# Kernel tuning notes

Hardware: AMD Instinct MI355X
Metric: run time of the kernel (lower is better)

## Reference

```python
import math
import jax, jax.numpy as jnp
import numpy as np

H = 8  # num_heads

def _layernorm(x, scale, bias, eps=1e-5):
    m = x.mean(-1, keepdims=True)
    v = x.var(-1, keepdims=True)
    return (x - m) / jnp.sqrt(v + eps) * scale + bias

def setup_inputs() -> dict:
    key = jax.random.key(0)
    ks = jax.random.split(key, 12)
    B, C, P, D, G = 8, 32, 256, 256, 512
    n = jax.random.normal
    return {
        "qz": n(ks[0], (B, C, P, D), dtype=jnp.float32),
        "unary": n(ks[1], (B, C, P, D), dtype=jnp.float32),
        # per-sample condition-instantiated factors; scaled ~1/sqrt(D) so attn logits are sane
        "time_u": n(ks[2], (B, D, D), dtype=jnp.float32) * 0.06,
        "time_v": n(ks[3], (B, D, D), dtype=jnp.float32) * 0.06,
        "channel_u": n(ks[4], (B, D, D), dtype=jnp.float32) * 0.06,
        "channel_v": n(ks[5], (B, D, D), dtype=jnp.float32) * 0.06,
        "topic_binary": n(ks[6], (B, G, D), dtype=jnp.float32) * 0.02,
        "norm_scale": jnp.ones((D,), jnp.float32),
        "norm_bias": jnp.zeros((D,), jnp.float32),
        "gate_w": n(ks[7], (D, D), dtype=jnp.float32) * 0.02,
        "gate_b": jnp.zeros((D,), jnp.float32),
        "out_w1": n(ks[8], (D, D), dtype=jnp.float32) * 0.02,
        "out_b1": jnp.zeros((D,), jnp.float32),
        "out_w2": n(ks[9], (D, D), dtype=jnp.float32) * 0.02,
        "out_b2": jnp.zeros((D,), jnp.float32),
    }

def reference(qz, unary, time_u, time_v, channel_u, channel_v, topic_binary,
              norm_scale, norm_bias, gate_w, gate_b, out_w1, out_b1, out_w2, out_b2):
    B, C, P, D = qz.shape
    R = D // H
    inv_sqrt_r = 1.0 / math.sqrt(R)

    qz_n = _layernorm(qz, norm_scale, norm_bias)

    def heads(x, w):  # [B,C,P,D] x [B,D,D] -> [B,C,P,H,R]
        return jnp.einsum('bcpd,bod->bcpo', x, w).reshape(B, C, P, H, R)

    # --- time-factor message: attention over P within each (b, c, h) ---
    qu = heads(qz_n, time_u).transpose(0, 1, 3, 2, 4)   # [B,C,H,P,R]
    qv = heads(qz_n, time_v).transpose(0, 1, 3, 2, 4)
    attn_t = jax.nn.softmax(jnp.einsum('bchpr,bchqr->bchpq', qu, qv) * inv_sqrt_r, axis=-1)
    m_t = jnp.einsum('bchpq,bcqd->bchpd', attn_t, qz_n).mean(axis=2)  # [B,C,P,D]

    # --- channel-factor message: attention over C within each (b, p, h) ---
    qu = heads(qz_n, channel_u).transpose(0, 2, 3, 1, 4)  # [B,P,H,C,R]
    qv = heads(qz_n, channel_v).transpose(0, 2, 3, 1, 4)
    attn_c = jax.nn.softmax(jnp.einsum('bphcr,bphfr->bphcf', qu, qv) * inv_sqrt_r, axis=-1)
    qzp = qz_n.transpose(0, 2, 1, 3)                      # [B,P,C,D]
    m_c = jnp.einsum('bphcf,bpfd->bphcd', attn_c, qzp).mean(axis=2).transpose(0, 2, 1, 3)

    # --- topic-modeling binary factor with AbsNormalize (relu + L1-normalize) ---
    qg = jax.nn.relu(jnp.einsum('bcpd,bgd->bcpg', qz_n, topic_binary))
    qg = qg / jnp.maximum(qg.sum(axis=-1, keepdims=True), 1e-6)
    m_g = jnp.einsum('bcpg,bgd->bcpd', qg, topic_binary)

    # --- gated residual update ---
    gate = jax.nn.sigmoid(qz @ gate_w.T + gate_b)
    qz2 = gate * qz + (1.0 - gate) * (unary + m_t + m_c + m_g)

    # --- output MLP with shared LayerNorm ---
    h = _layernorm(qz2, norm_scale, norm_bias)
    h = jax.nn.gelu(h @ out_w1.T + out_b1, approximate=False) @ out_w2.T + out_b2
    return qz2 + h
```

## Files before the change

### kernel.cpp

```cpp
#include <hip/hip_runtime.h>
#include <math.h>

namespace {

constexpr float INV_SQRT_R = 0.17677669529663689f;

typedef __attribute__((ext_vector_type(8))) __bf16 bf16x8;
typedef __attribute__((ext_vector_type(4))) float f32x4;

static __device__ __forceinline__ f32x4 MF(bf16x8 a, bf16x8 b, f32x4 c) {
    return __builtin_amdgcn_mfma_f32_16x16x32_bf16(a, b, c, 0, 0, 0);
}


__global__ __launch_bounds__(256) void prep_kernel(
    const float* __restrict__ time_u, const float* __restrict__ time_v,
    const float* __restrict__ chan_u, const float* __restrict__ chan_v,
    const float* __restrict__ topic, const float* __restrict__ gate_w,
    const float* __restrict__ w1, const float* __restrict__ w2,
    __bf16* __restrict__ wtime, __bf16* __restrict__ wchan,
    __bf16* __restrict__ topicFb, __bf16* __restrict__ topicTFb,
    __bf16* __restrict__ gwF, __bf16* __restrict__ w1F, __bf16* __restrict__ w2F)
{
    __shared__ __bf16 tile[32][34];
    const int blk = blockIdx.x;
    const int t = threadIdx.x;
    if (blk < 2048) {
        const int q = blk >> 9, r = blk & 511;
        const float* src; __bf16* dst; int dstOff;
        if (q == 0)      { src = time_u; dst = wtime; dstOff = 0; }
        else if (q == 1) { src = time_v; dst = wtime; dstOff = 65536; }
        else if (q == 2) { src = chan_u; dst = wchan; dstOff = 0; }
        else             { src = chan_v; dst = wchan; dstOff = 65536; }
        int i = (r * 256 + t) * 4;
        float4 v = *(const float4*)(src + i);
        int o = (i >> 16) * 131072 + dstOff + (i & 65535);
        dst[o + 0] = (__bf16)v.x; dst[o + 1] = (__bf16)v.y;
        dst[o + 2] = (__bf16)v.z; dst[o + 3] = (__bf16)v.w;
    } else if (blk < 3072) {
        int i = ((blk - 2048) * 256 + t) * 4;
        float4 v = *(const float4*)(topic + i);
        const int b = i >> 17, rem = i & 131071;
        const int g = rem >> 8, d = rem & 255;
        __bf16* dst = topicFb + (size_t)b * 131072 + (d >> 5) * 16384 + g * 32 + (d & 31);
        dst[0] = (__bf16)v.x; dst[1] = (__bf16)v.y; dst[2] = (__bf16)v.z; dst[3] = (__bf16)v.w;
    } else if (blk < 4096) {
        const int idx = blk - 3072;
        const int r0 = (idx & 15) * 32;
        const int c0 = ((idx >> 4) & 7) * 32;
        const size_t bz = idx >> 7;
        const float* src = topic + bz * 131072;
        __bf16* dst = topicTFb + bz * 131072;
        const int tx = t & 31, ty = t >> 5;
        #pragma unroll
        for (int i = 0; i < 32; i += 8)
            tile[ty + i][tx] = (__bf16)src[(size_t)(r0 + ty + i) * 256 + c0 + tx];
        __syncthreads();
        #pragma unroll
        for (int i = 0; i < 32; i += 8)
            dst[(r0 >> 5) * 8192 + (c0 + ty + i) * 32 + tx] = tile[tx][ty + i];
    } else {
        const int w = (blk - 4096) >> 6;
        const int r = (blk - 4096) & 63;
        const float* src = (w == 0) ? gate_w : ((w == 1) ? w1 : w2);
        __bf16* dstB = (w == 0) ? gwF : ((w == 1) ? w1F : w2F);
        int i = (r * 256 + t) * 4;
        float4 v = *(const float4*)(src + i);
        const int n = i >> 8, k = i & 255;
        __bf16* dst = dstB + (k >> 5) * 8192 + n * 32 + (k & 31);
        dst[0] = (__bf16)v.x; dst[1] = (__bf16)v.y; dst[2] = (__bf16)v.z; dst[3] = (__bf16)v.w;
    }
}

__global__ __launch_bounds__(256) void ln_kernel(
    const float* __restrict__ x, const float* __restrict__ sc,
    const float* __restrict__ bi, __bf16* __restrict__ y)
{
    const size_t row = blockIdx.x;
    const int t = threadIdx.x;
    const float v = x[row * 256 + t];
    float s = v, s2 = v * v;
    #pragma unroll
    for (int o = 32; o > 0; o >>= 1) {
        s  += __shfl_xor(s, o);
        s2 += __shfl_xor(s2, o);
    }
    __shared__ float ps[4], ps2[4];
    if ((t & 63) == 0) { ps[t >> 6] = s; ps2[t >> 6] = s2; }
    __syncthreads();
    const float S  = ps[0] + ps[1] + ps[2] + ps[3];
    const float S2 = ps2[0] + ps2[1] + ps2[2] + ps2[3];
    const float mean = S * (1.0f / 256.0f);
    const float var  = S2 * (1.0f / 256.0f) - mean * mean;
    const float inv  = 1.0f / sqrtf(var + 1e-5f);
    y[row * 256 + t] = (__bf16)((v - mean) * inv * sc[t] + bi[t]);
}

__global__ __launch_bounds__(256) void tpose_frag_kernel(
    const __bf16* __restrict__ src, __bf16* __restrict__ dst)
{
    const size_t bz = blockIdx.z;
    src += bz * 65536;
    dst += bz * 65536;
    __shared__ __bf16 tile[32][34];
    const int r0 = blockIdx.x * 32, c0 = blockIdx.y * 32;
    const int tx = threadIdx.x & 31, ty = threadIdx.x >> 5;
    #pragma unroll
    for (int i = 0; i < 32; i += 8)
        tile[ty + i][tx] = src[(size_t)(r0 + ty + i) * 256 + c0 + tx];
    __syncthreads();
    #pragma unroll
    for (int i = 0; i < 32; i += 8)
        dst[(r0 >> 5) * 8192 + (c0 + ty + i) * 32 + tx] = tile[tx][ty + i];
}

__global__ __launch_bounds__(256) void mgemm_kernel(
    const __bf16* __restrict__ A, const __bf16* __restrict__ Bm, __bf16* __restrict__ Cout,
    int K, size_t aStride, size_t bStride,
    size_t s_b, size_t s_c, size_t s_p, size_t s_w, size_t s_h)
{
    const int bb = blockIdx.z;
    const int m0 = blockIdx.x * 64;
    const int n0 = blockIdx.y * 256;
    const __bf16* Ab = A + (size_t)bb * aStride;
    const __bf16* Bb = Bm + (size_t)bb * bStride;
    __shared__ __align__(16) __bf16 As[64][40];
    __shared__ __align__(16) __bf16 Bs[256][40];
    const int t = threadIdx.x;
    const int lane = t & 63;
    const int wid = t >> 6;
    const int l15 = lane & 15, lg = lane >> 4;

    f32x4 acc[4][4] = {};

    for (int k0 = 0; k0 < K; k0 += 32) {
        {
            const int row = t >> 2, k8 = (t & 3) << 3;
            *(bf16x8*)&As[row][k8] = *(const bf16x8*)(Ab + (size_t)(m0 + row) * K + k0 + k8);
        }
        #pragma unroll
        for (int s = 0; s < 4; ++s) {
            const int slot = s * 256 + t;
            const int row = slot >> 2, k8 = (slot & 3) << 3;
            *(bf16x8*)&Bs[row][k8] = *(const bf16x8*)(Bb + (size_t)(n0 + row) * K + k0 + k8);
        }
        __syncthreads();
        bf16x8 af[4], bfr[4];
        #pragma unroll
        for (int i = 0; i < 4; ++i)
            af[i] = *(const bf16x8*)&As[i * 16 + l15][lg * 8];
        #pragma unroll
        for (int j = 0; j < 4; ++j)
            bfr[j] = *(const bf16x8*)&Bs[wid * 64 + j * 16 + l15][lg * 8];
        #pragma unroll
        for (int i = 0; i < 4; ++i)
            #pragma unroll
            for (int j = 0; j < 4; ++j)
                acc[i][j] = MF(af[i], bfr[j], acc[i][j]);
        __syncthreads();
    }

    #pragma unroll
    for (int j = 0; j < 4; ++j) {
        const int n = n0 + wid * 64 + j * 16 + l15;
        const size_t offn = (size_t)(n >> 8) * s_w + (size_t)((n >> 5) & 7) * s_h + (n & 31);
        #pragma unroll
        for (int i = 0; i < 4; ++i) {
            #pragma unroll
            for (int r = 0; r < 4; ++r) {
                const int m = m0 + i * 16 + lg * 4 + r;
                const size_t off = (size_t)bb * s_b + (size_t)(m >> 8) * s_c
                                 + (size_t)(m & 255) * s_p + offn;
                Cout[off] = (__bf16)acc[i][j][r];
            }
        }
    }
}

__global__ __launch_bounds__(256) void time_attn_mt_kernel(
    const __bf16* __restrict__ qu, const __bf16* __restrict__ qv,
    const __bf16* __restrict__ qznTF, __bf16* __restrict__ m_t)
{
    const int bc = blockIdx.x;
    const int p0 = blockIdx.y * 64;
    const __bf16* quB = qu + (size_t)bc * 65536;
    const __bf16* qvB = qv + (size_t)bc * 65536;
    const __bf16* BTF = qznTF + (size_t)bc * 65536;
    __shared__ __align__(16) __bf16 R1[16896];
    __bf16* Us  = R1;
    __bf16* Vs  = R1 + 2560;
    __bf16* aL  = R1;
    const int t = threadIdx.x;
    const int lane = t & 63;
    const int wid = t >> 6;
    const int l15 = lane & 15, lg = lane >> 4;

    f32x4 acc[16] = {};

    for (int h = 0; h < 8; ++h) {
        const __bf16* quH = quB + h * 8192;
        const __bf16* qvH = qvB + h * 8192;
        __syncthreads();
        {
            const int row = t >> 2, k8 = (t & 3) << 3;
            *(bf16x8*)&Us[row * 40 + k8] = *(const bf16x8*)(quH + (size_t)(p0 + row) * 32 + k8);
        }
        #pragma unroll
        for (int i = 0; i < 4; ++i) {
            const int slot = i * 256 + t;
            const int row = slot >> 2, k8 = (slot & 3) << 3;
            *(bf16x8*)&Vs[row * 40 + k8] = *(const bf16x8*)(qvH + (size_t)row * 32 + k8);
        }
        __syncthreads();

        f32x4 s[16];
        bf16x8 a = *(const bf16x8*)&Us[(wid * 16 + l15) * 40 + lg * 8];
        #pragma unroll
        for (int j = 0; j < 16; ++j) {
            bf16x8 bfr = *(const bf16x8*)&Vs[(j * 16 + l15) * 40 + lg * 8];
            s[j] = MF(a, bfr, (f32x4){0.f, 0.f, 0.f, 0.f});
        }

        #pragma unroll
        for (int r = 0; r < 4; ++r) {
            float e[16];
            float sum = 0.0f;
            #pragma unroll
            for (int j = 0; j < 16; ++j) {
                e[j] = __expf(s[j][r] * INV_SQRT_R);
                sum += e[j];
            }
            sum += __shfl_xor(sum, 1);
            sum += __shfl_xor(sum, 2);
            sum += __shfl_xor(sum, 4);
            sum += __shfl_xor(sum, 8);
            const float inv = 0.125f / sum;
            #pragma unroll
            for (int j = 0; j < 16; ++j) acc[j][r] += e[j] * inv;
        }
    }

    __syncthreads();
    #pragma unroll
    for (int r = 0; r < 4; ++r) {
        const int row = wid * 16 + lg * 4 + r;
        #pragma unroll
        for (int j = 0; j < 16; ++j)
            aL[row * 264 + j * 16 + l15] = (__bf16)acc[j][r];
    }
    __syncthreads();

    f32x4 acc2[4][4] = {};
    #pragma unroll
    for (int k0 = 0; k0 < 256; k0 += 32) {
        bf16x8 af[4], bfr[4];
        #pragma unroll
        for (int i = 0; i < 4; ++i)
            af[i] = *(const bf16x8*)&aL[(i * 16 + l15) * 264 + k0 + lg * 8];
        #pragma unroll
        for (int j = 0; j < 4; ++j)
            bfr[j] = *(const bf16x8*)(BTF + (k0 >> 5) * 8192 + (wid * 64 + j * 16 + l15) * 32 + lg * 8);
        #pragma unroll
        for (int i = 0; i < 4; ++i)
            #pragma unroll
            for (int j = 0; j < 4; ++j)
                acc2[i][j] = MF(af[i], bfr[j], acc2[i][j]);
    }
    #pragma unroll
    for (int i = 0; i < 4; ++i)
        #pragma unroll
        for (int j = 0; j < 4; ++j) {
            const int d = wid * 64 + j * 16 + l15;
            #pragma unroll
            for (int r = 0; r < 4; ++r) {
                const int p = p0 + i * 16 + lg * 4 + r;
                m_t[(size_t)bc * 65536 + (size_t)p * 256 + d] = (__bf16)acc2[i][j][r];
            }
        }
}

__global__ __launch_bounds__(256) void chan_fused_kernel(
    const __bf16* __restrict__ quc, const __bf16* __restrict__ qvc,
    const __bf16* __restrict__ qzn, __bf16* __restrict__ m_c)
{
    const int bp = blockIdx.x;
    const int b = bp >> 8, p = bp & 255;
    const __bf16* quB = quc + (size_t)bp * 8192;
    const __bf16* qvB = qvc + (size_t)bp * 8192;
    __shared__ __align__(16) __bf16 QU[20480];
    __shared__ float ab[32 * 33];
    __bf16* qus = QU;
    __bf16* qvs = QU + 10240;
    const int t = threadIdx.x;

    float btr[32];
    #pragma unroll
    for (int f = 0; f < 32; ++f)
        btr[f] = (float)qzn[((size_t)(b * 32 + f) * 256 + p) * 256 + t];

    #pragma unroll
    for (int i = 0; i < 4; ++i) {
        int fi = i * 256 + t;
        int e = fi << 3;
        int h = e >> 10, cc = (e >> 5) & 31, r = e & 31;
        int base = (h * 32 + cc) * 40 + r;
        *(bf16x8*)&qus[base] = *(const bf16x8*)(quB + e);
        *(bf16x8*)&qvs[base] = *(const bf16x8*)(qvB + e);
    }
    __syncthreads();
    const int c = t >> 3, j = t & 7;
    float acc[4] = {0.f, 0.f, 0.f, 0.f};
    for (int h = 0; h < 8; ++h) {
        float qur[32];
        #pragma unroll
        for (int u = 0; u < 4; ++u) {
            bf16x8 q8 = *(const bf16x8*)&qus[(h * 32 + c) * 40 + u * 8];
            #pragma unroll
            for (int e2 = 0; e2 < 8; ++e2) qur[u * 8 + e2] = (float)q8[e2];
        }
        float s[4];
        #pragma unroll
        for (int jj = 0; jj < 4; ++jj) {
            int f = j * 4 + jj;
            float a = 0.f;
            #pragma unroll
            for (int u = 0; u < 4; ++u) {
                bf16x8 v8 = *(const bf16x8*)&qvs[(h * 32 + f) * 40 + u * 8];
                #pragma unroll
                for (int e2 = 0; e2 < 8; ++e2) a += qur[u * 8 + e2] * (float)v8[e2];
            }
            s[jj] = a * INV_SQRT_R;
        }
        float mx = fmaxf(fmaxf(s[0], s[1]), fmaxf(s[2], s[3]));
        mx = fmaxf(mx, __shfl_xor(mx, 1));
        mx = fmaxf(mx, __shfl_xor(mx, 2));
        mx = fmaxf(mx, __shfl_xor(mx, 4));
        float e0x = __expf(s[0] - mx), e1x = __expf(s[1] - mx);
        float e2x = __expf(s[2] - mx), e3x = __expf(s[3] - mx);
        float sum = e0x + e1x + e2x + e3x;
        sum += __shfl_xor(sum, 1);
        sum += __shfl_xor(sum, 2);
        sum += __shfl_xor(sum, 4);
        float inv = 0.125f / sum;
        acc[0] += e0x * inv; acc[1] += e1x * inv; acc[2] += e2x * inv; acc[3] += e3x * inv;
    }
    #pragma unroll
    for (int jj = 0; jj < 4; ++jj) ab[c * 33 + j * 4 + jj] = acc[jj];
    __syncthreads();
    #pragma unroll 2
    for (int c2 = 0; c2 < 32; c2 += 2) {
        float a0 = 0.f, a1 = 0.f;
        #pragma unroll
        for (int f = 0; f < 32; ++f) {
            float v = btr[f];
            a0 += ab[c2 * 33 + f] * v;
            a1 += ab[(c2 + 1) * 33 + f] * v;
        }
        size_t off = ((size_t)(b * 32 + c2) * 256 + p) * 256 + t;
        m_c[off] = (__bf16)a0;
        m_c[off + 65536] = (__bf16)a1;
    }
}

__global__ __launch_bounds__(256) void topic_fused_kernel(
    const __bf16* __restrict__ qzn, const __bf16* __restrict__ topicFb,
    const __bf16* __restrict__ topicTFb, __bf16* __restrict__ m_g)
{
    const int bb = blockIdx.z;
    const int m0 = blockIdx.x * 32;
    const __bf16* Ab = qzn + (size_t)bb * 2097152;
    const __bf16* B1 = topicFb + (size_t)bb * 131072;
    const __bf16* B2 = topicTFb + (size_t)bb * 131072;
    __shared__ __align__(16) __bf16 As[32][264];
    __shared__ __align__(16) __bf16 Ps[32][520];
    __shared__ float rsInv[32];
    const int t = threadIdx.x;
    const int lane = t & 63, wid = t >> 6;
    const int l15 = lane & 15, lg = lane >> 4;

    #pragma unroll
    for (int s = 0; s < 4; ++s) {
        const int slot = s * 256 + t;
        const int row = slot >> 5, k8 = (slot & 31) << 3;
        *(bf16x8*)&As[row][k8] = *(const bf16x8*)(Ab + (size_t)(m0 + row) * 256 + k8);
    }
    __syncthreads();

    f32x4 acc[2][8] = {};
    #pragma unroll
    for (int k0 = 0; k0 < 256; k0 += 32) {
        bf16x8 af0 = *(const bf16x8*)&As[l15][k0 + lg * 8];
        bf16x8 af1 = *(const bf16x8*)&As[16 + l15][k0 + lg * 8];
        #pragma unroll
        for (int j = 0; j < 8; ++j) {
            bf16x8 b8 = *(const bf16x8*)(B1 + (k0 >> 5) * 16384 + (wid * 128 + j * 16 + l15) * 32 + lg * 8);
            acc[0][j] = MF(af0, b8, acc[0][j]);
            acc[1][j] = MF(af1, b8, acc[1][j]);
        }
    }
    #pragma unroll
    for (int i = 0; i < 2; ++i)
        #pragma unroll
        for (int j = 0; j < 8; ++j) {
            const int n = wid * 128 + j * 16 + l15;
            #pragma unroll
            for (int r = 0; r < 4; ++r)
                Ps[i * 16 + lg * 4 + r][n] = (__bf16)fmaxf(acc[i][j][r], 0.0f);
        }
    __syncthreads();
    {
        const int row = t >> 3, seg = t & 7;
        float s = 0.0f;
        #pragma unroll
        for (int u = 0; u < 8; ++u) {
            bf16x8 v = *(const bf16x8*)&Ps[row][seg * 64 + u * 8];
            #pragma unroll
            for (int e = 0; e < 8; ++e) s += (float)v[e];
        }
        s += __shfl_xor(s, 1);
        s += __shfl_xor(s, 2);
        s += __shfl_xor(s, 4);
        if (seg == 0) rsInv[row] = 1.0f / fmaxf(s, 1e-6f);
    }
    __syncthreads();
    f32x4 acc2[2][4] = {};
    #pragma unroll
    for (int k0 = 0; k0 < 512; k0 += 32) {
        bf16x8 af0 = *(const bf16x8*)&Ps[l15][k0 + lg * 8];
        bf16x8 af1 = *(const bf16x8*)&Ps[16 + l15][k0 + lg * 8];
        #pragma unroll
        for (int j = 0; j < 4; ++j) {
            bf16x8 b8 = *(const bf16x8*)(B2 + (k0 >> 5) * 8192 + (wid * 64 + j * 16 + l15) * 32 + lg * 8);
            acc2[0][j] = MF(af0, b8, acc2[0][j]);
            acc2[1][j] = MF(af1, b8, acc2[1][j]);
        }
    }
    #pragma unroll
    for (int i = 0; i < 2; ++i)
        #pragma unroll
        for (int j = 0; j < 4; ++j) {
            const int n = wid * 64 + j * 16 + l15;
            #pragma unroll
            for (int r = 0; r < 4; ++r) {
                const int ml = i * 16 + lg * 4 + r;
                m_g[(size_t)bb * 2097152 + (size_t)(m0 + ml) * 256 + n]
                    = (__bf16)(acc2[i][j][r] * rsInv[ml]);
            }
        }
}

__global__ __launch_bounds__(256) void mega_kernel(
    const float* __restrict__ qz, const float* __restrict__ unary,
    const __bf16* __restrict__ m_t, const __bf16* __restrict__ m_c,
    const __bf16* __restrict__ m_g,
    const __bf16* __restrict__ gwF, const float* __restrict__ gate_b,
    const __bf16* __restrict__ w1F, const float* __restrict__ b1,
    const __bf16* __restrict__ w2F, const float* __restrict__ b2,
    const float* __restrict__ nsc, const float* __restrict__ nbi,
    float* __restrict__ outp)
{
    const int m0 = blockIdx.x * 64;
    __shared__ __align__(16) __bf16 hL[64][264];
    __shared__ float lnp[64][8];
    const int t = threadIdx.x;
    const int lane = t & 63, wid = t >> 6;
    const int l15 = lane & 15, lg = lane >> 4;

    #pragma unroll
    for (int s = 0; s < 8; ++s) {
        const int slot = s * 256 + t;
        const int row = slot >> 5;
        const int k8 = (slot & 31) << 3;
        const float* src = qz + (size_t)(m0 + row) * 256 + k8;
        float4 v0 = *(const float4*)src;
        float4 v1 = *(const float4*)(src + 4);
        bf16x8 pk;
        pk[0] = (__bf16)v0.x; pk[1] = (__bf16)v0.y; pk[2] = (__bf16)v0.z; pk[3] = (__bf16)v0.w;
        pk[4] = (__bf16)v1.x; pk[5] = (__bf16)v1.y; pk[6] = (__bf16)v1.z; pk[7] = (__bf16)v1.w;
        *(bf16x8*)&hL[row][k8] = pk;
    }
    __syncthreads();

    f32x4 acc[4][4] = {};
    #pragma unroll
    for (int k0 = 0; k0 < 256; k0 += 32) {
        bf16x8 af[4], bfr[4];
        #pragma unroll
        for (int i = 0; i < 4; ++i) af[i] = *(const bf16x8*)&hL[i * 16 + l15][k0 + lg * 8];
        #pragma unroll
        for (int j = 0; j < 4; ++j)
            bfr[j] = *(const bf16x8*)(gwF + (k0 >> 5) * 8192 + (wid * 64 + j * 16 + l15) * 32 + lg * 8);
        #pragma unroll
        for (int i = 0; i < 4; ++i)
            #pragma unroll
            for (int j = 0; j < 4; ++j)
                acc[i][j] = MF(af[i], bfr[j], acc[i][j]);
    }

    f32x4 z2[4][4];
    #pragma unroll
    for (int i = 0; i < 4; ++i) {
        #pragma unroll
        for (int r = 0; r < 4; ++r) {
            const int rr = i * 16 + lg * 4 + r;
            float s = 0.0f, s2 = 0.0f;
            #pragma unroll
            for (int j = 0; j < 4; ++j) {
                const int n = wid * 64 + j * 16 + l15;
                const size_t off = (size_t)(m0 + rr) * 256 + n;
                float g = 1.0f / (1.0f + __expf(-(acc[i][j][r] + gate_b[n])));
                float rest = unary[off] + (float)m_t[off] + (float)m_c[off] + (float)m_g[off];
                float v = g * (float)hL[rr][n] + (1.0f - g) * rest;
                z2[i][j][r] = v;
                s += v; s2 += v * v;
            }
            s  += __shfl_xor(s, 1);  s  += __shfl_xor(s, 2);
            s  += __shfl_xor(s, 4);  s  += __shfl_xor(s, 8);
            s2 += __shfl_xor(s2, 1); s2 += __shfl_xor(s2, 2);
            s2 += __shfl_xor(s2, 4); s2 += __shfl_xor(s2, 8);
            if (l15 == 0) {
                lnp[rr][wid * 2 + 0] = s;
                lnp[rr][wid * 2 + 1] = s2;
            }
        }
    }
    __syncthreads();
    #pragma unroll
    for (int i = 0; i < 4; ++i) {
        #pragma unroll
        for (int r = 0; r < 4; ++r) {
            const int rr = i * 16 + lg * 4 + r;
            float S  = lnp[rr][0] + lnp[rr][2] + lnp[rr][4] + lnp[rr][6];
            float S2 = lnp[rr][1] + lnp[rr][3] + lnp[rr][5] + lnp[rr][7];
            float mean = S * (1.0f / 256.0f);
            float var  = S2 * (1.0f / 256.0f) - mean * mean;
            float inv  = 1.0f / sqrtf(var + 1e-5f);
            #pragma unroll
            for (int j = 0; j < 4; ++j) {
                const int n = wid * 64 + j * 16 + l15;
                hL[rr][n] = (__bf16)((z2[i][j][r] - mean) * inv * nsc[n] + nbi[n]);
            }
        }
    }
    __syncthreads();

    f32x4 acc2[4][4] = {};
    #pragma unroll
    for (int k0 = 0; k0 < 256; k0 += 32) {
        bf16x8 af[4], bfr[4];
        #pragma unroll
        for (int i = 0; i < 4; ++i) af[i] = *(const bf16x8*)&hL[i * 16 + l15][k0 + lg * 8];
        #pragma unroll
        for (int j = 0; j < 4; ++j)
            bfr[j] = *(const bf16x8*)(w1F + (k0 >> 5) * 8192 + (wid * 64 + j * 16 + l15) * 32 + lg * 8);
        #pragma unroll
        for (int i = 0; i < 4; ++i)
            #pragma unroll
            for (int j = 0; j < 4; ++j)
                acc2[i][j] = MF(af[i], bfr[j], acc2[i][j]);
    }
    __syncthreads();
    #pragma unroll
    for (int i = 0; i < 4; ++i)
        #pragma unroll
        for (int j = 0; j < 4; ++j) {
            const int n = wid * 64 + j * 16 + l15;
            const float bn = b1[n];
            #pragma unroll
            for (int r = 0; r < 4; ++r) {
                float x = acc2[i][j][r] + bn;
                hL[i * 16 + lg * 4 + r][n] = (__bf16)(0.5f * x * (1.0f + erff(x * 0.7071067811865475f)));
            }
        }
    __syncthreads();

    f32x4 acc3[4][4] = {};
    #pragma unroll
    for (int k0 = 0; k0 < 256; k0 += 32) {
        bf16x8 af[4], bfr[4];
        #pragma unroll
        for (int i = 0; i < 4; ++i) af[i] = *(const bf16x8*)&hL[i * 16 + l15][k0 + lg * 8];
        #pragma unroll
        for (int j = 0; j < 4; ++j)
            bfr[j] = *(const bf16x8*)(w2F + (k0 >> 5) * 8192 + (wid * 64 + j * 16 + l15) * 32 + lg * 8);
        #pragma unroll
        for (int i = 0; i < 4; ++i)
            #pragma unroll
            for (int j = 0; j < 4; ++j)
                acc3[i][j] = MF(af[i], bfr[j], acc3[i][j]);
    }
    #pragma unroll
    for (int i = 0; i < 4; ++i)
        #pragma unroll
        for (int j = 0; j < 4; ++j) {
            const int n = wid * 64 + j * 16 + l15;
            const float bn = b2[n];
            #pragma unroll
            for (int r = 0; r < 4; ++r) {
                const size_t off = (size_t)(m0 + i * 16 + lg * 4 + r) * 256 + n;
                outp[off] = z2[i][j][r] + acc3[i][j][r] + bn;
            }
        }
}

}

extern "C" void kernel_launch(void* const* d_in, const int* in_sizes, int n_in,
                              void* d_out, int out_size, void* d_ws, size_t ws_size,
                              hipStream_t stream)
{
    (void)in_sizes; (void)n_in; (void)out_size; (void)ws_size;
    const float* qz     = (const float*)d_in[0];
    const float* unary  = (const float*)d_in[1];
    const float* time_u = (const float*)d_in[2];
    const float* time_v = (const float*)d_in[3];
    const float* chan_u = (const float*)d_in[4];
    const float* chan_v = (const float*)d_in[5];
    const float* topic  = (const float*)d_in[6];
    const float* nsc    = (const float*)d_in[7];
    const float* nbi    = (const float*)d_in[8];
    const float* gate_w = (const float*)d_in[9];
    const float* gate_b = (const float*)d_in[10];
    const float* w1     = (const float*)d_in[11];
    const float* b1     = (const float*)d_in[12];
    const float* w2     = (const float*)d_in[13];
    const float* b2     = (const float*)d_in[14];

    char* base = (char*)d_ws;
    __bf16* qzn_b  = (__bf16*)base;
    __bf16* pool   = (__bf16*)(base + (32ull << 20));
    __bf16* wtime  = pool;
    __bf16* wchan  = pool + 1048576;
    __bf16* topicFb = pool + 2097152;
    __bf16* topicTFb= pool + 3145728;
    __bf16* gwF    = pool + 4194304;
    __bf16* w1F    = pool + 4259840;
    __bf16* w2F    = pool + 4325376;
    __bf16* Blo    = (__bf16*)(base + (64ull << 20));
    __bf16* Bhi    = (__bf16*)(base + (96ull << 20));
    __bf16* qu_t   = Blo;
    __bf16* qv_t   = Bhi;
    __bf16* qu_c   = Blo;
    __bf16* qv_c   = Bhi;
    __bf16* m_g    = Blo;
    __bf16* qznTF  = (__bf16*)(base + (128ull << 20));
    __bf16* m_c    = qznTF;
    __bf16* m_t    = (__bf16*)(base + (160ull << 20));
    float*  OUTF   = (float*)d_out;

    dim3 blk(256);

    prep_kernel<<<4288, blk, 0, stream>>>(
        time_u, time_v, chan_u, chan_v, topic, gate_w, w1, w2,
        wtime, wchan, topicFb, topicTFb, gwF, w1F, w2F);

    ln_kernel<<<65536, blk, 0, stream>>>(qz, nsc, nbi, qzn_b);
    tpose_frag_kernel<<<dim3(8, 8, 256), blk, 0, stream>>>(qzn_b, qznTF);

    mgemm_kernel<<<dim3(128, 2, 8), blk, 0, stream>>>(
        qzn_b, wtime, qu_t, 256, 2097152, 131072,
        2097152, 65536, 32, 16777216, 8192);

    time_attn_mt_kernel<<<dim3(256, 4), blk, 0, stream>>>(qu_t, qv_t, qznTF, m_t);

    mgemm_kernel<<<dim3(128, 2, 8), blk, 0, stream>>>(
        qzn_b, wchan, qu_c, 256, 2097152, 131072,
        2097152, 32, 8192, 16777216, 1024);

    chan_fused_kernel<<<2048, blk, 0, stream>>>(qu_c, qv_c, qzn_b, m_c);

    topic_fused_kernel<<<dim3(256, 1, 8), blk, 0, stream>>>(qzn_b, topicFb, topicTFb, m_g);

    mega_kernel<<<1024, blk, 0, stream>>>(
        qz, unary, m_t, m_c, m_g,
        gwF, gate_b, w1F, b1, w2F, b2, nsc, nbi, OUTF);
}
```

Baseline: 530.6 us.

## Stage topic GEMM B tiles through LDS with plain row-major topic layouts

The topic kernel now loads per-k-step tiles of the topic matrix (and its transpose) cooperatively into shared memory, then reads MFMA fragments from LDS instead of gathering them straight from global memory in a pre-fragmented layout. The prep kernel writes plain row-major bf16 copies instead. A launch bound of 2 blocks per SM is added. This aims at more coalesced global loads, at the cost of extra barriers per k-step, about 40KB more LDS per block, and no double buffering.

Result: faster. 483.6 us (median of 4 runs) (-8.9%).

```diff
diff --git a/kernel.cpp b/kernel.cpp
--- a/kernel.cpp
+++ b/kernel.cpp
@@ -19,7 +19,7 @@
     const float* __restrict__ topic, const float* __restrict__ gate_w,
     const float* __restrict__ w1, const float* __restrict__ w2,
     __bf16* __restrict__ wtime, __bf16* __restrict__ wchan,
-    __bf16* __restrict__ topicFb, __bf16* __restrict__ topicTFb,
+    __bf16* __restrict__ topicb, __bf16* __restrict__ topicTb,
     __bf16* __restrict__ gwF, __bf16* __restrict__ w1F, __bf16* __restrict__ w2F)
 {
     __shared__ __bf16 tile[32][34];
@@ -40,17 +40,15 @@
     } else if (blk < 3072) {
         int i = ((blk - 2048) * 256 + t) * 4;
         float4 v = *(const float4*)(topic + i);
-        const int b = i >> 17, rem = i & 131071;
-        const int g = rem >> 8, d = rem & 255;
-        __bf16* dst = topicFb + (size_t)b * 131072 + (d >> 5) * 16384 + g * 32 + (d & 31);
-        dst[0] = (__bf16)v.x; dst[1] = (__bf16)v.y; dst[2] = (__bf16)v.z; dst[3] = (__bf16)v.w;
+        topicb[i + 0] = (__bf16)v.x; topicb[i + 1] = (__bf16)v.y;
+        topicb[i + 2] = (__bf16)v.z; topicb[i + 3] = (__bf16)v.w;
     } else if (blk < 4096) {
         const int idx = blk - 3072;
         const int r0 = (idx & 15) * 32;
         const int c0 = ((idx >> 4) & 7) * 32;
         const size_t bz = idx >> 7;
         const float* src = topic + bz * 131072;
-        __bf16* dst = topicTFb + bz * 131072;
+        __bf16* dst = topicTb + bz * 131072;
         const int tx = t & 31, ty = t >> 5;
         #pragma unroll
         for (int i = 0; i < 32; i += 8)
@@ -58,7 +56,7 @@
         __syncthreads();
         #pragma unroll
         for (int i = 0; i < 32; i += 8)
-            dst[(r0 >> 5) * 8192 + (c0 + ty + i) * 32 + tx] = tile[tx][ty + i];
+            dst[(size_t)(c0 + ty + i) * 512 + r0 + tx] = tile[tx][ty + i];
     } else {
         const int w = (blk - 4096) >> 6;
         const int r = (blk - 4096) & 63;
@@ -362,41 +360,45 @@
     }
 }
 
-__global__ __launch_bounds__(256) void topic_fused_kernel(
-    const __bf16* __restrict__ qzn, const __bf16* __restrict__ topicFb,
-    const __bf16* __restrict__ topicTFb, __bf16* __restrict__ m_g)
+__global__ __launch_bounds__(256, 2) void topic_fused_kernel(
+    const __bf16* __restrict__ qzn, const __bf16* __restrict__ topicb,
+    const __bf16* __restrict__ topicTb, __bf16* __restrict__ m_g)
 {
     const int bb = blockIdx.z;
     const int m0 = blockIdx.x * 32;
     const __bf16* Ab = qzn + (size_t)bb * 2097152;
-    const __bf16* B1 = topicFb + (size_t)bb * 131072;
-    const __bf16* B2 = topicTFb + (size_t)bb * 131072;
-    __shared__ __align__(16) __bf16 As[32][264];
+    const __bf16* B1 = topicb + (size_t)bb * 131072;
+    const __bf16* B2 = topicTb + (size_t)bb * 131072;
+    __shared__ __align__(16) __bf16 As[32][40];
+    __shared__ __align__(16) __bf16 Bs[512][40];
     __shared__ __align__(16) __bf16 Ps[32][520];
     __shared__ float rsInv[32];
     const int t = threadIdx.x;
     const int lane = t & 63, wid = t >> 6;
     const int l15 = lane & 15, lg = lane >> 4;
 
-    #pragma unroll
-    for (int s = 0; s < 4; ++s) {
-        const int slot = s * 256 + t;
-        const int row = slot >> 5, k8 = (slot & 31) << 3;
-        *(bf16x8*)&As[row][k8] = *(const bf16x8*)(Ab + (size_t)(m0 + row) * 256 + k8);
-    }
-    __syncthreads();
-
     f32x4 acc[2][8] = {};
-    #pragma unroll
     for (int k0 = 0; k0 < 256; k0 += 32) {
-        bf16x8 af0 = *(const bf16x8*)&As[l15][k0 + lg * 8];
-        bf16x8 af1 = *(const bf16x8*)&As[16 + l15][k0 + lg * 8];
+        if (t < 128) {
+            const int row = t >> 2, k8 = (t & 3) << 3;
+            *(bf16x8*)&As[row][k8] = *(const bf16x8*)(Ab + (size_t)(m0 + row) * 256 + k0 + k8);
+        }
+        #pragma unroll
+        for (int s = 0; s < 8; ++s) {
+            const int slot = s * 256 + t;
+            const int row = slot >> 2, k8 = (slot & 3) << 3;
+            *(bf16x8*)&Bs[row][k8] = *(const bf16x8*)(B1 + (size_t)row * 256 + k0 + k8);
+        }
+        __syncthreads();
+        bf16x8 af0 = *(const bf16x8*)&As[l15][lg * 8];
+        bf16x8 af1 = *(const bf16x8*)&As[16 + l15][lg * 8];
         #pragma unroll
         for (int j = 0; j < 8; ++j) {
-            bf16x8 b8 = *(const bf16x8*)(B1 + (k0 >> 5) * 16384 + (wid * 128 + j * 16 + l15) * 32 + lg * 8);
+            bf16x8 b8 = *(const bf16x8*)&Bs[wid * 128 + j * 16 + l15][lg * 8];
             acc[0][j] = MF(af0, b8, acc[0][j]);
             acc[1][j] = MF(af1, b8, acc[1][j]);
         }
+        __syncthreads();
     }
     #pragma unroll
     for (int i = 0; i < 2; ++i)
@@ -424,16 +426,23 @@
     }
     __syncthreads();
     f32x4 acc2[2][4] = {};
-    #pragma unroll
     for (int k0 = 0; k0 < 512; k0 += 32) {
+        #pragma unroll
+        for (int s = 0; s < 4; ++s) {
+            const int slot = s * 256 + t;
+            const int row = slot >> 2, k8 = (slot & 3) << 3;
+            *(bf16x8*)&Bs[row][k8] = *(const bf16x8*)(B2 + (size_t)row * 512 + k0 + k8);
+        }
+        __syncthreads();
         bf16x8 af0 = *(const bf16x8*)&Ps[l15][k0 + lg * 8];
         bf16x8 af1 = *(const bf16x8*)&Ps[16 + l15][k0 + lg * 8];
         #pragma unroll
         for (int j = 0; j < 4; ++j) {
-            bf16x8 b8 = *(const bf16x8*)(B2 + (k0 >> 5) * 8192 + (wid * 64 + j * 16 + l15) * 32 + lg * 8);
+            bf16x8 b8 = *(const bf16x8*)&Bs[wid * 64 + j * 16 + l15][lg * 8];
             acc2[0][j] = MF(af0, b8, acc2[0][j]);
             acc2[1][j] = MF(af1, b8, acc2[1][j]);
         }
+        __syncthreads();
     }
     #pragma unroll
     for (int i = 0; i < 2; ++i)
@@ -631,8 +640,8 @@
     __bf16* pool   = (__bf16*)(base + (32ull << 20));
     __bf16* wtime  = pool;
     __bf16* wchan  = pool + 1048576;
-    __bf16* topicFb = pool + 2097152;
-    __bf16* topicTFb= pool + 3145728;
+    __bf16* topicb = pool + 2097152;
+    __bf16* topicTb= pool + 3145728;
     __bf16* gwF    = pool + 4194304;
     __bf16* w1F    = pool + 4259840;
     __bf16* w2F    = pool + 4325376;
@@ -652,7 +661,7 @@
 
     prep_kernel<<<4288, blk, 0, stream>>>(
         time_u, time_v, chan_u, chan_v, topic, gate_w, w1, w2,
-        wtime, wchan, topicFb, topicTFb, gwF, w1F, w2F);
+        wtime, wchan, topicb, topicTb, gwF, w1F, w2F);
 
     ln_kernel<<<65536, blk, 0, stream>>>(qz, nsc, nbi, qzn_b);
     tpose_frag_kernel<<<dim3(8, 8, 256), blk, 0, stream>>>(qzn_b, qznTF);
@@ -669,7 +678,7 @@
 
     chan_fused_kernel<<<2048, blk, 0, stream>>>(qu_c, qv_c, qzn_b, m_c);
 
-    topic_fused_kernel<<<dim3(256, 1, 8), blk, 0, stream>>>(qzn_b, topicFb, topicTFb, m_g);
+    topic_fused_kernel<<<dim3(256, 1, 8), blk, 0, stream>>>(qzn_b, topicb, topicTb, m_g);
 
     mega_kernel<<<1024, blk, 0, stream>>>(
         qz, unary, m_t, m_c, m_g,
```
